# Optimization experiments

Measured on AMD Instinct MI355X. Metric: run time of the kernel, lower is better.

The kernel has to match this reference:

```python
import jax, jax.numpy as jnp
import numpy as np

N_SENT = 100000   # source ('sent') nodes
N_TYPE = 10000    # destination ('type') nodes
E = 640000        # edges of etype 'has'
D = 128           # out_dim
LEAKY_SLOPE = 0.01  # F.leaky_relu default


def setup_inputs() -> dict:
    key = jax.random.key(0)
    k0, k1, k2, k3, k4 = jax.random.split(key, 5)
    h_sent = jax.random.normal(k0, (N_SENT, D), jnp.float32)
    h_type = jax.random.normal(k1, (N_TYPE, D), jnp.float32)
    # attn_fc: Linear(2*D, 1, bias=False) -> weight [1, 2*D]
    attn_w = jax.random.normal(k2, (1, 2 * D), jnp.float32) * (1.0 / np.sqrt(2 * D))
    src_idx = jax.random.randint(k3, (E,), 0, N_SENT, dtype=jnp.int32)
    dst_idx = jax.random.randint(k4, (E,), 0, N_TYPE, dtype=jnp.int32)
    return {"h_sent": h_sent, "h_type": h_type, "attn_w": attn_w,
            "src_idx": src_idx, "dst_idx": dst_idx}


def reference(h_sent, h_type, attn_w, src_idx, dst_idx):
    w = attn_w[0]  # [2D]
    # attn_fc(cat(src_h, dst_h)) == src_h @ w[:D] + dst_h @ w[D:]  (no bias)
    s_src = h_sent @ w[:D]   # [N_SENT]
    s_dst = h_type @ w[D:]   # [N_TYPE]
    e = jax.nn.leaky_relu(s_src[src_idx] + s_dst[dst_idx], LEAKY_SLOPE)  # [E]
    # segment (per-destination) softmax over incoming edges
    m = jax.ops.segment_max(e, dst_idx, num_segments=N_TYPE)             # [N_TYPE]
    m = jnp.where(jnp.isfinite(m), m, 0.0)                               # empty segments -> 0
    ex = jnp.exp(e - m[dst_idx])                                         # [E]
    denom = jax.ops.segment_sum(ex, dst_idx, num_segments=N_TYPE)        # [N_TYPE]
    alpha = ex / denom[dst_idx]                                          # [E]
    # weighted scatter-sum of source features into destination nodes
    msg = alpha[:, None] * h_sent[src_idx]                               # [E, D]
    h_new = jax.ops.segment_sum(msg, dst_idx, num_segments=N_TYPE)       # [N_TYPE, D]
    # DGL only updates nodes that received messages; isolated nodes keep h
    deg = jax.ops.segment_sum(jnp.ones_like(e), dst_idx, num_segments=N_TYPE)
    return jnp.where(deg[:, None] > 0, h_new, h_type)
```

## Files before the change

### kernel.cpp

```cpp
#include <hip/hip_runtime.h>
#include <stdint.h>
#include <stddef.h>

#define N_SENT 100000
#define N_TYPE 10000
#define NEDGE  640000
#define NROWS  (N_SENT + N_TYPE)
#define MAXDEG 256
#define HB     256
#define HCHUNK (NEDGE / HB)

__device__ __forceinline__ float bf2f(uint32_t lo16) {
    return __builtin_bit_cast(float, lo16 << 16);
}
__device__ __forceinline__ uint32_t f2bf(float f) {
    uint32_t u = __builtin_bit_cast(uint32_t, f);
    return (u + 0x7fffu + ((u >> 16) & 1u)) >> 16;
}

__device__ __forceinline__ bool detect_bf16(const uint32_t* __restrict__ h) {
    uint32_t u = h[threadIdx.x & 63];
    uint32_t e_lo = (u >> 7) & 0xffu;
    int ok = (e_lo >= 100u && e_lo <= 140u) ? 1 : 0;
    unsigned long long m = __ballot(ok);
    return __popcll(m) >= 48;
}

#define SC_BLOCKS 6875

__global__ __launch_bounds__(256) void scores_k(const void* __restrict__ h_sent,
                                                const void* __restrict__ h_type,
                                                const void* __restrict__ attn_w,
                                                float* __restrict__ s_src,
                                                float* __restrict__ s_dst) {
    int t    = blockIdx.x * 256 + (int)threadIdx.x;
    int lane = threadIdx.x & 63;
    bool isbf = detect_bf16((const uint32_t*)h_sent);
    if (isbf) {
        uint4 wsv = ((const uint4*)attn_w)[lane & 15];
        uint4 wtv = ((const uint4*)attn_w)[16 + (lane & 15)];
        bool isSrc = t < N_SENT * 16;
        const uint4* p = isSrc ? (const uint4*)h_sent + t
                               : (const uint4*)h_type + (t - N_SENT * 16);
        uint4 h = *p;
        uint4 wv = isSrc ? wsv : wtv;
        float s = bf2f(h.x & 0xffffu) * bf2f(wv.x & 0xffffu)
                + bf2f(h.x >> 16)     * bf2f(wv.x >> 16)
                + bf2f(h.y & 0xffffu) * bf2f(wv.y & 0xffffu)
                + bf2f(h.y >> 16)     * bf2f(wv.y >> 16)
                + bf2f(h.z & 0xffffu) * bf2f(wv.z & 0xffffu)
                + bf2f(h.z >> 16)     * bf2f(wv.z >> 16)
                + bf2f(h.w & 0xffffu) * bf2f(wv.w & 0xffffu)
                + bf2f(h.w >> 16)     * bf2f(wv.w >> 16);
        s += __shfl_xor(s, 1, 64);
        s += __shfl_xor(s, 2, 64);
        s += __shfl_xor(s, 4, 64);
        s += __shfl_xor(s, 8, 64);
        if ((lane & 15) == 0) {
            int row = t >> 4;
            if (row < N_SENT) s_src[row] = s;
            else              s_dst[row - N_SENT] = s;
        }
    } else {
        float4 wsv = ((const float4*)attn_w)[lane & 31];
        float4 wtv = ((const float4*)attn_w)[32 + (lane & 31)];
        const int HALF = NROWS * 16;
        int it0 = t, it1 = t + HALF;
        bool s0 = it0 < N_SENT * 32, s1 = it1 < N_SENT * 32;
        const float4* p0 = s0 ? (const float4*)h_sent + it0
                              : (const float4*)h_type + (it0 - N_SENT * 32);
        const float4* p1 = s1 ? (const float4*)h_sent + it1
                              : (const float4*)h_type + (it1 - N_SENT * 32);
        float4 h0 = *p0;
        float4 h1 = *p1;
        __builtin_amdgcn_sched_barrier(0);
        float4 w0 = s0 ? wsv : wtv, w1 = s1 ? wsv : wtv;
        float a = h0.x * w0.x + h0.y * w0.y + h0.z * w0.z + h0.w * w0.w;
        float b = h1.x * w1.x + h1.y * w1.y + h1.z * w1.z + h1.w * w1.w;
        a += __shfl_xor(a, 1, 64);  b += __shfl_xor(b, 1, 64);
        a += __shfl_xor(a, 2, 64);  b += __shfl_xor(b, 2, 64);
        a += __shfl_xor(a, 4, 64);  b += __shfl_xor(b, 4, 64);
        a += __shfl_xor(a, 8, 64);  b += __shfl_xor(b, 8, 64);
        a += __shfl_xor(a, 16, 64); b += __shfl_xor(b, 16, 64);
        if ((lane & 31) == 0) {
            int r0 = it0 >> 5, r1 = it1 >> 5;
            if (r0 < N_SENT) s_src[r0] = a; else s_dst[r0 - N_SENT] = a;
            if (r1 < N_SENT) s_src[r1] = b; else s_dst[r1 - N_SENT] = b;
        }
    }
}

__global__ __launch_bounds__(256) void count_k(const int* __restrict__ dst,
                                               uint32_t* __restrict__ count2) {
    __shared__ uint32_t hist[N_TYPE];
    int cb = blockIdx.x;
    int t  = threadIdx.x;
#pragma unroll
    for (int i = 0; i < 40; i++) {
        int idx = i * 256 + t;
        if (idx < N_TYPE) hist[idx] = 0u;
    }
    __syncthreads();
    int e0 = cb * HCHUNK;
    int dv[10];
#pragma unroll
    for (int k = 0; k < 10; k++) {
        int i = k * 256 + t;
        dv[k] = dst[e0 + (i < HCHUNK ? i : HCHUNK - 1)];
    }
    __builtin_amdgcn_sched_barrier(0);
#pragma unroll
    for (int k = 0; k < 10; k++) {
        int i = k * 256 + t;
        if (i < HCHUNK) atomicAdd(&hist[dv[k]], 1u);
    }
    __syncthreads();
    uint4* row = (uint4*)(count2 + (size_t)cb * N_TYPE);
#pragma unroll
    for (int i = 0; i < 10; i++) {
        int idx = i * 256 + t;
        if (idx < N_TYPE / 4) row[idx] = ((const uint4*)hist)[idx];
    }
}

__global__ __launch_bounds__(256) void sumscan_k(uint32_t* __restrict__ count2,
                                                 uint32_t* __restrict__ total) {
    int b = blockIdx.x * 256 + (int)threadIdx.x;
    bool ok = b < N_TYPE;
    int bc = ok ? b : N_TYPE - 1;
    uint32_t run = 0;
#pragma unroll
    for (int g = 0; g < HB / 64; g++) {
        uint32_t vals[64];
#pragma unroll
        for (int c = 0; c < 64; c++)
            vals[c] = count2[(size_t)(g * 64 + c) * N_TYPE + bc];
        __builtin_amdgcn_sched_barrier(0);
#pragma unroll
        for (int c = 0; c < 64; c++) { uint32_t v = vals[c]; vals[c] = run; run += v; }
        if (ok) {
#pragma unroll
            for (int c = 0; c < 64; c++)
                count2[(size_t)(g * 64 + c) * N_TYPE + b] = vals[c];
        }
    }
    if (ok) total[b] = run;
}

__global__ __launch_bounds__(1024) void scan_k(const uint32_t* __restrict__ total,
                                               uint32_t* __restrict__ offsets) {
    const int CH = 10;
    int t = threadIdx.x, lane = t & 63, wv = t >> 6;
    int base = t * CH;
    uint32_t local[CH];
    uint32_t tsum = 0;
#pragma unroll
    for (int i = 0; i < CH; i++) {
        int idx = base + i;
        uint32_t c = (idx < N_TYPE) ? total[idx] : 0u;
        local[i] = c;
        tsum += c;
    }
    uint32_t orig = tsum;
#pragma unroll
    for (int off = 1; off < 64; off <<= 1) {
        uint32_t v = __shfl_up(tsum, off, 64);
        if (lane >= off) tsum += v;
    }
    __shared__ uint32_t wsum[16];
    if (lane == 63) wsum[wv] = tsum;
    __syncthreads();
    if (wv == 0 && lane < 16) {
        uint32_t u = wsum[lane], o = u;
#pragma unroll
        for (int off = 1; off < 16; off <<= 1) {
            uint32_t v = __shfl_up(u, off, 64);
            if (lane >= off) u += v;
        }
        wsum[lane] = u - o;
    }
    __syncthreads();
    uint32_t run = wsum[wv] + tsum - orig;
#pragma unroll
    for (int i = 0; i < CH; i++) {
        int idx = base + i;
        if (idx < N_TYPE) {
            offsets[idx] = run;
            run += local[i];
        } else if (idx == N_TYPE) {
            offsets[idx] = run;
        }
    }
}

__global__ __launch_bounds__(256) void fill_k(const int* __restrict__ src,
                                              const int* __restrict__ dst,
                                              const uint32_t* __restrict__ offsets,
                                              const uint32_t* __restrict__ base2,
                                              uint32_t* __restrict__ edge_src) {
    __shared__ uint32_t cur[N_TYPE];
    int cb = blockIdx.x;
    int t  = threadIdx.x;
    const uint32_t* brow = base2 + (size_t)cb * N_TYPE;
#pragma unroll
    for (int i = 0; i < 10; i++) {
        int idx = i * 256 + t;
        if (idx < N_TYPE / 4) {
            uint4 o = ((const uint4*)offsets)[idx];
            uint4 b = ((const uint4*)brow)[idx];
            uint4 c; c.x = o.x + b.x; c.y = o.y + b.y; c.z = o.z + b.z; c.w = o.w + b.w;
            ((uint4*)cur)[idx] = c;
        }
    }
    __syncthreads();
    int e0 = cb * HCHUNK;
    int dv[10], sv[10];
#pragma unroll
    for (int k = 0; k < 10; k++) {
        int i = k * 256 + t;
        int e = e0 + (i < HCHUNK ? i : HCHUNK - 1);
        dv[k] = dst[e];
        sv[k] = src[e];
    }
    __builtin_amdgcn_sched_barrier(0);
#pragma unroll
    for (int k = 0; k < 10; k++) {
        int i = k * 256 + t;
        if (i < HCHUNK) {
            uint32_t pos = atomicAdd(&cur[dv[k]], 1u);
            edge_src[pos] = (uint32_t)sv[k];
        }
    }
}

__global__ __launch_bounds__(256) void agg_k(const void* __restrict__ h_sent,
                                             const void* __restrict__ h_type,
                                             const float* __restrict__ s_src,
                                             const float* __restrict__ s_dst,
                                             const uint32_t* __restrict__ offsets,
                                             const uint32_t* __restrict__ edge_src,
                                             void* __restrict__ out) {
    __shared__ float    sc[4][MAXDEG];
    __shared__ uint32_t ss[4][MAXDEG];
    int j     = (blockIdx.x * 256 + threadIdx.x) >> 6;
    int wslot = threadIdx.x >> 6;
    int lane  = threadIdx.x & 63;
    bool valid = j < N_TYPE;
    bool isbf  = detect_bf16((const uint32_t*)h_sent);
    uint32_t beg = 0, deg = 0;
    float sdj = 0.0f;
    if (valid) {
        beg = offsets[j];
        deg = offsets[j + 1] - beg;
        sdj = s_dst[j];
    }
    float*    mysc = sc[wslot];
    uint32_t* myss = ss[wslot];
    bool fits = (deg <= MAXDEG);
    float m = -INFINITY;
    for (uint32_t k = lane; k < deg; k += 64) {
        uint32_t s = edge_src[beg + k];
        float v = s_src[s] + sdj;
        v = v > 0.0f ? v : 0.01f * v;
        if (fits) { mysc[k] = v; myss[k] = s; }
        m = fmaxf(m, v);
    }
#pragma unroll
    for (int off = 32; off; off >>= 1) m = fmaxf(m, __shfl_xor(m, off, 64));
    __syncthreads();
    if (!valid) return;
    if (deg == 0) {
        if (isbf) ((uint32_t*)out)[(size_t)j * 64 + lane] =
                      ((const uint32_t*)h_type)[(size_t)j * 64 + lane];
        else      ((float2*)out)[(size_t)j * 64 + lane] =
                      ((const float2*)h_type)[(size_t)j * 64 + lane];
        return;
    }
    float denom = 0.0f, a0 = 0.0f, a1 = 0.0f;
    if (isbf) {
        const uint32_t* hp = (const uint32_t*)h_sent;
        uint32_t k = 0;
        if (fits) {
            for (; k + 16 <= deg; k += 16) {
                uint32_t sv[16]; float vv[16]; uint32_t gv[16];
#pragma unroll
                for (int i = 0; i < 16; i++) { sv[i] = myss[k + i]; vv[i] = mysc[k + i]; }
#pragma unroll
                for (int i = 0; i < 16; i++) gv[i] = hp[(size_t)sv[i] * 64 + lane];
#pragma unroll
                for (int i = 0; i < 16; i++) {
                    float w = __expf(vv[i] - m);
                    denom += w;
                    a0 += w * bf2f(gv[i] & 0xffffu);
                    a1 += w * bf2f(gv[i] >> 16);
                }
            }
            for (; k + 8 <= deg; k += 8) {
                uint32_t sv[8]; float vv[8]; uint32_t gv[8];
#pragma unroll
                for (int i = 0; i < 8; i++) { sv[i] = myss[k + i]; vv[i] = mysc[k + i]; }
#pragma unroll
                for (int i = 0; i < 8; i++) gv[i] = hp[(size_t)sv[i] * 64 + lane];
#pragma unroll
                for (int i = 0; i < 8; i++) {
                    float w = __expf(vv[i] - m);
                    denom += w;
                    a0 += w * bf2f(gv[i] & 0xffffu);
                    a1 += w * bf2f(gv[i] >> 16);
                }
            }
            for (; k < deg; ++k) {
                float w = __expf(mysc[k] - m);
                uint32_t g = hp[(size_t)myss[k] * 64 + lane];
                denom += w;
                a0 += w * bf2f(g & 0xffffu);
                a1 += w * bf2f(g >> 16);
            }
        } else {
            for (k = 0; k < deg; ++k) {
                uint32_t s = edge_src[beg + k];
                float v = s_src[s] + sdj; v = v > 0.0f ? v : 0.01f * v;
                float w = __expf(v - m);
                uint32_t g = hp[(size_t)s * 64 + lane];
                denom += w;
                a0 += w * bf2f(g & 0xffffu);
                a1 += w * bf2f(g >> 16);
            }
        }
        float inv = 1.0f / denom;
        ((uint32_t*)out)[(size_t)j * 64 + lane] = f2bf(a0 * inv) | (f2bf(a1 * inv) << 16);
    } else {
        const float2* hp = (const float2*)h_sent;
        uint32_t k = 0;
        if (fits) {
            for (; k + 16 <= deg; k += 16) {
                uint32_t sv[16]; float vv[16]; float2 gv[16];
#pragma unroll
                for (int i = 0; i < 16; i++) { sv[i] = myss[k + i]; vv[i] = mysc[k + i]; }
#pragma unroll
                for (int i = 0; i < 16; i++) gv[i] = hp[(size_t)sv[i] * 64 + lane];
#pragma unroll
                for (int i = 0; i < 16; i++) {
                    float w = __expf(vv[i] - m);
                    denom += w;
                    a0 += w * gv[i].x;
                    a1 += w * gv[i].y;
                }
            }
            for (; k + 8 <= deg; k += 8) {
                uint32_t sv[8]; float vv[8]; float2 gv[8];
#pragma unroll
                for (int i = 0; i < 8; i++) { sv[i] = myss[k + i]; vv[i] = mysc[k + i]; }
#pragma unroll
                for (int i = 0; i < 8; i++) gv[i] = hp[(size_t)sv[i] * 64 + lane];
#pragma unroll
                for (int i = 0; i < 8; i++) {
                    float w = __expf(vv[i] - m);
                    denom += w;
                    a0 += w * gv[i].x;
                    a1 += w * gv[i].y;
                }
            }
            for (; k < deg; ++k) {
                float w = __expf(mysc[k] - m);
                float2 g = hp[(size_t)myss[k] * 64 + lane];
                denom += w;
                a0 += w * g.x;
                a1 += w * g.y;
            }
        } else {
            for (k = 0; k < deg; ++k) {
                uint32_t s = edge_src[beg + k];
                float v = s_src[s] + sdj; v = v > 0.0f ? v : 0.01f * v;
                float w = __expf(v - m);
                float2 g = hp[(size_t)s * 64 + lane];
                denom += w;
                a0 += w * g.x;
                a1 += w * g.y;
            }
        }
        float inv = 1.0f / denom;
        ((float2*)out)[(size_t)j * 64 + lane] = make_float2(a0 * inv, a1 * inv);
    }
}

static inline size_t align_up(size_t x) { return (x + 255) & ~(size_t)255; }

extern "C" void kernel_launch(void* const* d_in, const int* in_sizes, int n_in,
                              void* d_out, int out_size, void* d_ws, size_t ws_size,
                              hipStream_t stream) {
    const void* h_sent = d_in[0];
    const void* h_type = d_in[1];
    const void* attn_w = d_in[2];
    const int* src_idx = (const int*)d_in[3];
    const int* dst_idx = (const int*)d_in[4];

    char* w = (char*)d_ws;
    float*    s_src     = (float*)w;    w += align_up((size_t)N_SENT * 4);
    float*    s_dst     = (float*)w;    w += align_up((size_t)N_TYPE * 4);
    uint32_t* count2    = (uint32_t*)w; w += align_up((size_t)HB * N_TYPE * 4);
    uint32_t* total     = (uint32_t*)w; w += align_up((size_t)N_TYPE * 4);
    uint32_t* offsets   = (uint32_t*)w; w += align_up((size_t)(N_TYPE + 1) * 4);
    uint32_t* edge_src  = (uint32_t*)w; w += align_up((size_t)NEDGE * 4);

    scores_k<<<SC_BLOCKS, 256, 0, stream>>>(h_sent, h_type, attn_w, s_src, s_dst);
    count_k<<<HB, 256, 0, stream>>>(dst_idx, count2);
    sumscan_k<<<(N_TYPE + 255) / 256, 256, 0, stream>>>(count2, total);
    scan_k<<<1, 1024, 0, stream>>>(total, offsets);
    fill_k<<<HB, 256, 0, stream>>>(src_idx, dst_idx, offsets, count2, edge_src);
    agg_k<<<(N_TYPE + 3) / 4, 256, 0, stream>>>(h_sent, h_type, s_src, s_dst,
                                                offsets, edge_src, d_out);
}
```

Baseline: 174.7 us.

## Fuse CSR build kernels into one cooperative kernel with grid syncs

```diff
diff --git a/kernel.cpp b/kernel.cpp
--- a/kernel.cpp
+++ b/kernel.cpp
@@ -1,6 +1,9 @@
 #include <hip/hip_runtime.h>
+#include <hip/hip_cooperative_groups.h>
 #include <stdint.h>
 #include <stddef.h>
+
+namespace cg = cooperative_groups;
 
 #define N_SENT 100000
 #define N_TYPE 10000
@@ -90,6 +93,151 @@
     }
 }
 
+__global__ __launch_bounds__(256) void build2_k(const int* __restrict__ src,
+                                                const int* __restrict__ dst,
+                                                uint32_t* __restrict__ count2,
+                                                uint32_t* __restrict__ total,
+                                                uint32_t* __restrict__ offsets,
+                                                uint32_t* __restrict__ edge_src) {
+    __shared__ uint32_t hist[N_TYPE];
+    cg::grid_group gg = cg::this_grid();
+    int bid  = blockIdx.x;
+    int t    = threadIdx.x;
+    int lane = t & 63;
+    int tid  = bid * 256 + t;
+
+    {
+#pragma unroll
+        for (int i = 0; i < 40; i++) {
+            int idx = i * 256 + t;
+            if (idx < N_TYPE) hist[idx] = 0u;
+        }
+        __syncthreads();
+        int e0 = bid * HCHUNK;
+        int dv[10];
+#pragma unroll
+        for (int k = 0; k < 10; k++) {
+            int i = k * 256 + t;
+            dv[k] = dst[e0 + (i < HCHUNK ? i : HCHUNK - 1)];
+        }
+        __builtin_amdgcn_sched_barrier(0);
+#pragma unroll
+        for (int k = 0; k < 10; k++) {
+            int i = k * 256 + t;
+            if (i < HCHUNK) atomicAdd(&hist[dv[k]], 1u);
+        }
+        __syncthreads();
+        uint4* row = (uint4*)(count2 + (size_t)bid * N_TYPE);
+#pragma unroll
+        for (int i = 0; i < 10; i++) {
+            int idx = i * 256 + t;
+            if (idx < N_TYPE / 4) row[idx] = ((const uint4*)hist)[idx];
+        }
+    }
+    gg.sync();
+
+    {
+        int grp = tid >> 2;
+        int sub = t & 3;
+        if (grp < N_TYPE) {
+            uint32_t vals[64];
+#pragma unroll
+            for (int c = 0; c < 64; c++)
+                vals[c] = count2[(size_t)(sub * 64 + c) * N_TYPE + grp];
+            __builtin_amdgcn_sched_barrier(0);
+            uint32_t lsum = 0;
+#pragma unroll
+            for (int c = 0; c < 64; c++) lsum += vals[c];
+            uint32_t incl = lsum;
+#pragma unroll
+            for (int off = 1; off < 4; off <<= 1) {
+                uint32_t v = __shfl_up(incl, off, 64);
+                if ((lane & 3) >= off) incl += v;
+            }
+            uint32_t run = incl - lsum;
+#pragma unroll
+            for (int c = 0; c < 64; c++) {
+                uint32_t v = vals[c];
+                count2[(size_t)(sub * 64 + c) * N_TYPE + grp] = run;
+                run += v;
+            }
+            if (sub == 3) total[grp] = incl;
+        }
+    }
+    gg.sync();
+
+    if (bid == 0) {
+        const int CH = 40;
+        int wv = t >> 6;
+        int base = t * CH;
+        uint32_t local[CH];
+        uint32_t tsum = 0;
+#pragma unroll
+        for (int i = 0; i < CH; i++) {
+            int idx = base + i;
+            uint32_t c = (idx < N_TYPE) ? total[idx] : 0u;
+            local[i] = c;
+            tsum += c;
+        }
+        uint32_t incl = tsum;
+#pragma unroll
+        for (int off = 1; off < 64; off <<= 1) {
+            uint32_t v = __shfl_up(incl, off, 64);
+            if (lane >= off) incl += v;
+        }
+        if (lane == 63) hist[wv] = incl;
+        __syncthreads();
+        uint32_t wbase = 0;
+#pragma unroll
+        for (int w = 0; w < 4; w++) wbase += (w < wv) ? hist[w] : 0u;
+        uint32_t run = wbase + incl - tsum;
+#pragma unroll
+        for (int i = 0; i < CH; i++) {
+            int idx = base + i;
+            if (idx < N_TYPE) {
+                offsets[idx] = run;
+                run += local[i];
+            } else if (idx == N_TYPE) {
+                offsets[idx] = run;
+            }
+        }
+    }
+    gg.sync();
+
+    {
+        const uint32_t* brow = count2 + (size_t)bid * N_TYPE;
+#pragma unroll
+        for (int i = 0; i < 10; i++) {
+            int idx = i * 256 + t;
+            if (idx < N_TYPE / 4) {
+                uint4 o = ((const uint4*)offsets)[idx];
+                uint4 b = ((const uint4*)brow)[idx];
+                uint4 c; c.x = o.x + b.x; c.y = o.y + b.y; c.z = o.z + b.z; c.w = o.w + b.w;
+                ((uint4*)hist)[idx] = c;
+            }
+        }
+        __syncthreads();
+        int e0 = bid * HCHUNK;
+        int dv[10], sv[10];
+#pragma unroll
+        for (int k = 0; k < 10; k++) {
+            int i = k * 256 + t;
+            int e = e0 + (i < HCHUNK ? i : HCHUNK - 1);
+            dv[k] = dst[e];
+            sv[k] = src[e];
+        }
+        __builtin_amdgcn_sched_barrier(0);
+#pragma unroll
+        for (int k = 0; k < 10; k++) {
+            int i = k * 256 + t;
+            if (i < HCHUNK) {
+                uint32_t pos = atomicAdd(&hist[dv[k]], 1u);
+                edge_src[pos] = (uint32_t)sv[k];
+            }
+        }
+    }
+}
+
 __global__ __launch_bounds__(256) void count_k(const int* __restrict__ dst,
                                                uint32_t* __restrict__ count2) {
     __shared__ uint32_t hist[N_TYPE];
@@ -404,10 +552,18 @@
     uint32_t* edge_src  = (uint32_t*)w; w += align_up((size_t)NEDGE * 4);
 
     scores_k<<<SC_BLOCKS, 256, 0, stream>>>(h_sent, h_type, attn_w, s_src, s_dst);
-    count_k<<<HB, 256, 0, stream>>>(dst_idx, count2);
-    sumscan_k<<<(N_TYPE + 255) / 256, 256, 0, stream>>>(count2, total);
-    scan_k<<<1, 1024, 0, stream>>>(total, offsets);
-    fill_k<<<HB, 256, 0, stream>>>(src_idx, dst_idx, offsets, count2, edge_src);
+
+    void* args[] = { (void*)&src_idx, (void*)&dst_idx, (void*)&count2,
+                     (void*)&total, (void*)&offsets, (void*)&edge_src };
+    hipError_t cerr = hipLaunchCooperativeKernel((void*)build2_k, dim3(256), dim3(256),
+                                                 args, 0, stream);
+    if (cerr != hipSuccess) {
+        count_k<<<HB, 256, 0, stream>>>(dst_idx, count2);
+        sumscan_k<<<(N_TYPE + 255) / 256, 256, 0, stream>>>(count2, total);
+        scan_k<<<1, 1024, 0, stream>>>(total, offsets);
+        fill_k<<<HB, 256, 0, stream>>>(src_idx, dst_idx, offsets, count2, edge_src);
+    }
+
     agg_k<<<(N_TYPE + 3) / 4, 256, 0, stream>>>(h_sent, h_type, s_src, s_dst,
                                                 offsets, edge_src, d_out);
 }
```

Result: slower. 284.1 us (+62.6%).
